# Kernel tuning notes

Measured on AMD Instinct MI355X. Metric: run time of the kernel, lower is better.

## Reference

```python
import jax, jax.numpy as jnp
import numpy as np

B, S, IN, H, NH, PF, L = 8, 1024, 256, 1024, 16, 4096, 6
HD = H // NH
EPS = 1e-5


def _layernorm(x, g, b):
    m = jnp.mean(x, axis=-1, keepdims=True)
    v = jnp.mean((x - m) ** 2, axis=-1, keepdims=True)
    return (x - m) * jax.lax.rsqrt(v + EPS) * g + b


def setup_inputs() -> dict:
    key = jax.random.key(0)
    ks = iter(jax.random.split(key, 40))
    sd = 0.02
    inp = {
        "input_x": jax.random.normal(next(ks), (B, S, IN), jnp.float32),
        "emb_W": jax.random.normal(next(ks), (IN, H), jnp.float32) * sd,
        "emb_b": jnp.zeros((H,), jnp.float32),
        "pos_tab": jax.random.normal(next(ks), (S, H), jnp.float32) * sd,
        "Wq": jax.random.normal(next(ks), (L, H, H), jnp.float32) * sd,
        "bq": jnp.zeros((L, H), jnp.float32),
        "Wk": jax.random.normal(next(ks), (L, H, H), jnp.float32) * sd,
        "bk": jnp.zeros((L, H), jnp.float32),
        "Wv": jax.random.normal(next(ks), (L, H, H), jnp.float32) * sd,
        "bv": jnp.zeros((L, H), jnp.float32),
        "Wo": jax.random.normal(next(ks), (L, H, H), jnp.float32) * sd,
        "bo": jnp.zeros((L, H), jnp.float32),
        "ln1_g": jnp.ones((L, H), jnp.float32),
        "ln1_b": jnp.zeros((L, H), jnp.float32),
        "W1": jax.random.normal(next(ks), (L, H, PF), jnp.float32) * sd,
        "b1": jnp.zeros((L, PF), jnp.float32),
        "W2": jax.random.normal(next(ks), (L, PF, H), jnp.float32) * sd,
        "b2": jnp.zeros((L, H), jnp.float32),
        "ln2_g": jnp.ones((L, H), jnp.float32),
        "ln2_b": jnp.zeros((L, H), jnp.float32),
    }
    return inp


def _encoder(input_x, emb_W, emb_b, pos_tab, Wq, bq, Wk, bk, Wv, bv, Wo, bo,
             ln1_g, ln1_b, W1, b1, W2, b2, ln2_g, ln2_b):
    scale = jnp.sqrt(jnp.float32(H))  # module scales by sqrt(hidden_size)
    x = (input_x @ emb_W + emb_b) * scale + pos_tab[None, :, :]  # [B,S,H]

    def layer(x, p):
        wq, bq_, wk, bk_, wv, bv_, wo, bo_, g1, be1, w1, b1_, w2, b2_, g2, be2 = p
        q = (x @ wq + bq_).reshape(B, S, NH, HD).transpose(0, 2, 1, 3)  # bhsd
        k = (x @ wk + bk_).reshape(B, S, NH, HD).transpose(0, 2, 1, 3)
        v = (x @ wv + bv_).reshape(B, S, NH, HD).transpose(0, 2, 1, 3)
        energy = jnp.einsum("bhqd,bhkd->bhqk", q, k) / scale  # NOTE: /sqrt(H)
        attn = jax.nn.softmax(energy, axis=-1)
        o = jnp.einsum("bhqk,bhkd->bhqd", attn, v)
        o = o.transpose(0, 2, 1, 3).reshape(B, S, H) @ wo + bo_
        x = _layernorm(x + o, g1, be1)
        f = jax.nn.relu(x @ w1 + b1_) @ w2 + b2_
        x = _layernorm(x + f, g2, be2)
        return x, None

    params = (Wq, bq, Wk, bk, Wv, bv, Wo, bo, ln1_g, ln1_b, W1, b1, W2, b2, ln2_g, ln2_b)
    x, _ = jax.lax.scan(layer, x, params)
    return x


def reference(input_x, emb_W, emb_b, pos_tab, Wq, bq, Wk, bk, Wv, bv, Wo, bo,
              ln1_g, ln1_b, W1, b1, W2, b2, ln2_g, ln2_b):
    return _encoder(input_x, emb_W, emb_b, pos_tab, Wq, bq, Wk, bk, Wv, bv,
                    Wo, bo, ln1_g, ln1_b, W1, b1, W2, b2, ln2_g, ln2_b)
```

## Files before the change

kernel.cpp:

```cpp
#include <hip/hip_runtime.h>

#define HDIM 1024
#define BB 8
#define SS 1024
#define NHEAD 16
#define PFF 4096
#define NLAYER 6
#define MM (BB*SS)

typedef __attribute__((ext_vector_type(8))) short bf16x8_t;
typedef __attribute__((ext_vector_type(4))) float f32x4_t;
typedef __attribute__((ext_vector_type(16))) float f32x16_t;

static __device__ __forceinline__ unsigned short f2b(float f) {
  unsigned int u = __float_as_uint(f);
  u += 0x7fffu + ((u >> 16) & 1u);
  return (unsigned short)(u >> 16);
}

static __device__ __forceinline__ unsigned pkbf(float lo, float hi) {
  unsigned r;
  asm("v_cvt_pk_bf16_f32 %0, %1, %2" : "=v"(r) : "v"(lo), "v"(hi));
  return r;
}

static __device__ __forceinline__ bf16x8_t mk8(unsigned a, unsigned b, unsigned c, unsigned d) {
  union { unsigned u[4]; bf16x8_t v; } x;
  x.u[0] = a; x.u[1] = b; x.u[2] = c; x.u[3] = d;
  return x.v;
}

static __device__ __forceinline__ void gload16(const void* g, void* l) {
  __builtin_amdgcn_global_load_lds((__attribute__((address_space(1))) void*)g,
                                   (__attribute__((address_space(3))) void*)l, 16, 0, 0);
}

template<int N>
static __device__ __forceinline__ void vwait() {
  asm volatile("s_waitcnt vmcnt(%0)" :: "n"(N) : "memory");
}

static __device__ __forceinline__ void bar() {
  asm volatile("" ::: "memory");
  __builtin_amdgcn_s_barrier();
  asm volatile("" ::: "memory");
}

__global__ __launch_bounds__(256) void cvt_bf16(const float* __restrict__ in,
                                                unsigned short* __restrict__ o, int n4) {
  const int i = blockIdx.x * 256 + threadIdx.x;
  if (i < n4) {
    const float4 v = ((const float4*)in)[i];
    ushort4 ob = { f2b(v.x), f2b(v.y), f2b(v.z), f2b(v.w) };
    ((ushort4*)o)[i] = ob;
  }
}

__global__ __launch_bounds__(256) void transpose_bf16(const float* __restrict__ in,
                                                      unsigned short* __restrict__ outT,
                                                      int R, int C) {
  __shared__ float tile[32][33];
  const int c0 = blockIdx.x * 32, r0 = blockIdx.y * 32;
  const int tx = threadIdx.x, ty = threadIdx.y;
#pragma unroll
  for (int i = 0; i < 4; ++i)
    tile[ty + 8*i][tx] = in[(size_t)(r0 + ty + 8*i) * C + c0 + tx];
  __syncthreads();
#pragma unroll
  for (int i = 0; i < 4; ++i)
    outT[(size_t)(c0 + ty + 8*i) * R + r0 + tx] = f2b(tile[tx][ty + 8*i]);
}

__global__ __launch_bounds__(256) void vtrans(const unsigned short* __restrict__ qkv,
                                              unsigned short* __restrict__ vt) {
  __shared__ unsigned short tile[32][34];
  const int s0 = blockIdx.x * 32;
  const int by = blockIdx.y;
  const int bh = by >> 1, dt = by & 1;
  const int b = bh >> 4, h = bh & 15;
  const int tx = threadIdx.x, ty = threadIdx.y;
  const unsigned short* src = qkv + ((size_t)(b * 1024 + s0)) * 3072 + 2048 + h * 64 + dt * 32;
#pragma unroll
  for (int i = 0; i < 4; ++i)
    tile[ty + 8*i][tx] = src[(size_t)(ty + 8*i) * 3072 + tx];
  __syncthreads();
  unsigned short* dst = vt + (size_t)(bh * 64 + dt * 32) * 1024 + s0;
#pragma unroll
  for (int i = 0; i < 4; ++i)
    dst[(size_t)(ty + 8*i) * 1024 + tx] = tile[tx][ty + 8*i];
}

__global__ __launch_bounds__(256) void concat_bias(const float* __restrict__ bq,
                                                   const float* __restrict__ bk,
                                                   const float* __restrict__ bv,
                                                   float* __restrict__ o) {
  const int i = blockIdx.x * 256 + threadIdx.x;
  o[i] = (i < 1024) ? bq[i] : ((i < 2048) ? bk[i - 1024] : bv[i - 2048]);
}

template<int BN, bool BIAS, bool RELU, bool RESID, bool EMB, bool WF32, bool WBF16>
__global__ __launch_bounds__(512, 2) void gemm2c(
    const unsigned short* __restrict__ A,
    const unsigned short* __restrict__ Bt,
    const float* __restrict__ bias,
    const float* __restrict__ resid,
    const float* __restrict__ pos,
    float* __restrict__ outf,
    unsigned short* __restrict__ outb,
    int M, int N, int K) {
  constexpr int NJ = BN / 64;
  constexpr int WCN = BN / 4;
  constexpr int BUFSZ = 32768 + BN * 128;
  __shared__ __align__(1024) char smem[2 * BUFSZ];
  const int t = threadIdx.x, lane = t & 63, w = t >> 6;
  const int wr = w >> 2, wc = w & 3;

  int flat = blockIdx.x + gridDim.x * blockIdx.y;
  const int cpx = (gridDim.x * gridDim.y) >> 3;
  flat = (flat & 7) * cpx + (flat >> 3);
  const int m0 = (flat / gridDim.x) * 256;
  const int n0 = (flat % gridDim.x) * BN;

  const f32x4_t z = {0.f, 0.f, 0.f, 0.f};
  f32x4_t acc[8][NJ];
#pragma unroll
  for (int i = 0; i < 8; ++i)
#pragma unroll
    for (int j = 0; j < NJ; ++j) acc[i][j] = z;

  auto stageA = [&](int i, int kt, int buf) {
    const int chunk = i * 8 + w;
    const int byteoff = chunk * 1024 + lane * 16;
    const int row = byteoff >> 7;
    const int scb = (byteoff & 127) ^ ((row & 7) << 4);
    gload16((const char*)A + ((size_t)(m0 + row) * K + (kt << 6)) * 2 + scb,
            smem + buf * BUFSZ + chunk * 1024);
  };
  auto stageB = [&](int i, int kt, int buf) {
    const int chunk = i * 8 + w;
    const int byteoff = chunk * 1024 + lane * 16;
    const int row = byteoff >> 7;
    const int scb = (byteoff & 127) ^ ((row & 7) << 4);
    gload16((const char*)Bt + ((size_t)(n0 + row) * K + (kt << 6)) * 2 + scb,
            smem + buf * BUFSZ + 32768 + chunk * 1024);
  };
  auto readA = [&](const char* ab, int fi, int ks) {
    const int row = wr * 128 + fi * 16 + (lane & 15);
    const int cb = ks * 64 + ((lane >> 4) << 4);
    return *(const bf16x8_t*)(ab + row * 128 + (cb ^ ((row & 7) << 4)));
  };
  auto readB = [&](const char* bb, int j, int ks) {
    const int row = wc * WCN + j * 16 + (lane & 15);
    const int cb = ks * 64 + ((lane >> 4) << 4);
    return *(const bf16x8_t*)(bb + row * 128 + (cb ^ ((row & 7) << 4)));
  };

  stageB(0, 0, 0); stageB(1, 0, 0);
  if constexpr (NJ >= 3) stageB(2, 0, 0);
  if constexpr (NJ >= 4) stageB(3, 0, 0);
  stageA(0, 0, 0); stageA(2, 0, 0); stageA(1, 0, 0); stageA(3, 0, 0);

  const int nkt = K >> 6;
  for (int kt = 0; kt < nkt; ++kt) {
    const char* ab = smem + (kt & 1) * BUFSZ;
    const char* bb = ab + 32768;
    const int nb = (kt & 1) ^ 1;
    const bool pf = (kt + 1 < nkt);
    bf16x8_t bfr[NJ][2], af[8][2];

    if constexpr (BN >= 192) {
      vwait<2>(); bar();
      if (pf) { stageB(0, kt + 1, nb); stageB(1, kt + 1, nb); }
#pragma unroll
      for (int j = 0; j < NJ; ++j)
#pragma unroll
        for (int ks = 0; ks < 2; ++ks) bfr[j][ks] = readB(bb, j, ks);
#pragma unroll
      for (int d = 0; d < 4; ++d)
#pragma unroll
        for (int ks = 0; ks < 2; ++ks) af[d][ks] = readA(ab, d, ks);
      __builtin_amdgcn_s_setprio(1);
#pragma unroll
      for (int ks = 0; ks < 2; ++ks)
#pragma unroll
        for (int d = 0; d < 2; ++d)
#pragma unroll
          for (int j = 0; j < NJ; ++j)
            acc[d][j] = __builtin_amdgcn_mfma_f32_16x16x32_bf16(af[d][ks], bfr[j][ks], acc[d][j], 0, 0, 0);
      __builtin_amdgcn_s_setprio(0);
      if (pf) vwait<2>(); else vwait<0>();
      bar();
      if (pf) {
        stageB(2, kt + 1, nb);
        if constexpr (NJ >= 4) stageB(3, kt + 1, nb);
        stageA(0, kt + 1, nb);
      }
#pragma unroll
      for (int d = 4; d < 6; ++d)
#pragma unroll
        for (int ks = 0; ks < 2; ++ks) af[d][ks] = readA(ab, d, ks);
      __builtin_amdgcn_s_setprio(1);
#pragma unroll
      for (int ks = 0; ks < 2; ++ks)
#pragma unroll
        for (int d = 2; d < 4; ++d)
#pragma unroll
          for (int j = 0; j < NJ; ++j)
            acc[d][j] = __builtin_amdgcn_mfma_f32_16x16x32_bf16(af[d][ks], bfr[j][ks], acc[d][j], 0, 0, 0);
      __builtin_amdgcn_s_setprio(0);
      if (pf) stageA(2, kt + 1, nb);
#pragma unroll
      for (int d = 6; d < 8; ++d)
#pragma unroll
        for (int ks = 0; ks < 2; ++ks) af[d][ks] = readA(ab, d, ks);
      __builtin_amdgcn_s_setprio(1);
#pragma unroll
      for (int ks = 0; ks < 2; ++ks)
#pragma unroll
        for (int d = 4; d < 6; ++d)
#pragma unroll
          for (int j = 0; j < NJ; ++j)
            acc[d][j] = __builtin_amdgcn_mfma_f32_16x16x32_bf16(af[d][ks], bfr[j][ks], acc[d][j], 0, 0, 0);
      __builtin_amdgcn_s_setprio(0);
      if (pf) { stageA(1, kt + 1, nb); stageA(3, kt + 1, nb); }
      __builtin_amdgcn_s_setprio(1);
#pragma unroll
      for (int ks = 0; ks < 2; ++ks)
#pragma unroll
        for (int d = 6; d < 8; ++d)
#pragma unroll
          for (int j = 0; j < NJ; ++j)
            acc[d][j] = __builtin_amdgcn_mfma_f32_16x16x32_bf16(af[d][ks], bfr[j][ks], acc[d][j], 0, 0, 0);
      __builtin_amdgcn_s_setprio(0);
    } else {
      vwait<2>(); bar();
      if (pf) { stageB(0, kt + 1, nb); stageB(1, kt + 1, nb); stageA(0, kt + 1, nb); }
#pragma unroll
      for (int j = 0; j < NJ; ++j)
#pragma unroll
        for (int ks = 0; ks < 2; ++ks) bfr[j][ks] = readB(bb, j, ks);
#pragma unroll
      for (int d = 0; d < 4; ++d)
#pragma unroll
        for (int ks = 0; ks < 2; ++ks) af[d][ks] = readA(ab, d, ks);
      __builtin_amdgcn_s_setprio(1);
#pragma unroll
      for (int ks = 0; ks < 2; ++ks)
#pragma unroll
        for (int d = 0; d < 4; ++d)
#pragma unroll
          for (int j = 0; j < NJ; ++j)
            acc[d][j] = __builtin_amdgcn_mfma_f32_16x16x32_bf16(af[d][ks], bfr[j][ks], acc[d][j], 0, 0, 0);
      __builtin_amdgcn_s_setprio(0);
      if (pf) vwait<3>(); else vwait<0>();
      bar();
      if (pf) { stageA(2, kt + 1, nb); stageA(1, kt + 1, nb); stageA(3, kt + 1, nb); }
#pragma unroll
      for (int d = 4; d < 8; ++d)
#pragma unroll
        for (int ks = 0; ks < 2; ++ks) af[d][ks] = readA(ab, d, ks);
      __builtin_amdgcn_s_setprio(1);
#pragma unroll
      for (int ks = 0; ks < 2; ++ks)
#pragma unroll
        for (int d = 4; d < 8; ++d)
#pragma unroll
          for (int j = 0; j < NJ; ++j)
            acc[4 > d ? 0 : d][j] = __builtin_amdgcn_mfma_f32_16x16x32_bf16(af[d][ks], bfr[j][ks], acc[d][j], 0, 0, 0);
      __builtin_amdgcn_s_setprio(0);
    }
  }

#pragma unroll
  for (int i = 0; i < 8; ++i) {
    const int rbase = m0 + wr * 128 + i * 16 + ((lane >> 4) << 2);
#pragma unroll
    for (int j = 0; j < NJ; ++j) {
      const int cc = n0 + wc * WCN + j * 16 + (lane & 15);
      float bv = 0.f;
      if (BIAS) bv = bias[cc];
#pragma unroll
      for (int r = 0; r < 4; ++r) {
        const int row = rbase + r;
        float v = acc[i][j][r] + bv;
        if (EMB)  v = v * 32.f + pos[(size_t)(row & (SS - 1)) * N + cc];
        if (RELU) v = fmaxf(v, 0.f);
        if (RESID) v += resid[(size_t)row * N + cc];
        if (WF32)  outf[(size_t)row * N + cc] = v;
        if (WBF16) outb[(size_t)row * N + cc] = f2b(v);
      }
    }
  }
}

__global__ __launch_bounds__(256) void attn2(
    const unsigned short* __restrict__ qkv,
    const unsigned short* __restrict__ vt,
    unsigned short* __restrict__ O) {
  __shared__ __align__(1024) char smem[2 * 16384];
  const int t = threadIdx.x, lane = t & 63, w = t >> 6;
  const int l31 = lane & 31, lg = lane >> 5;
  const int bh = blockIdx.y;
  const int b = bh >> 4, h = bh & 15;
  const size_t rowb = (size_t)b << 10;
  const int q0 = blockIdx.x * 128 + w * 32;

  bf16x8_t qf[4];
  {
    const unsigned short* Qp = qkv + (rowb + q0 + l31) * 3072 + h * 64 + lg * 8;
#pragma unroll
    for (int dd = 0; dd < 4; ++dd) qf[dd] = *(const bf16x8_t*)(Qp + dd * 16);
  }

  f32x16_t oa0, oa1;
#pragma unroll
  for (int r = 0; r < 16; ++r) { oa0[r] = 0.f; oa1[r] = 0.f; }
  float m_run = -1e30f, l_run = 0.f;
  const float inv32 = 1.f / 32.f;

  const char* kglob = (const char*)qkv + ((size_t)1024 + h * 64) * 2;
  const char* vglob = (const char*)vt + (size_t)bh * 64 * 1024 * 2;

  auto stage = [&](int kt, int buf) {
    char* kbuf = smem + buf * 16384;
    char* vbuf = kbuf + 8192;
#pragma unroll
    for (int i = 0; i < 2; ++i) {
      const int chunk = w * 2 + i;
      const int byteoff = chunk * 1024 + lane * 16;
      const int row = byteoff >> 7;
      const int scb = (byteoff & 127) ^ ((row & 7) << 4);
      gload16(kglob + (size_t)(rowb + kt * 64 + row) * 6144 + scb, kbuf + chunk * 1024);
      gload16(vglob + ((size_t)row * 1024 + kt * 64) * 2 + scb,    vbuf + chunk * 1024);
    }
  };

  stage(0, 0);
  for (int kt = 0; kt < 16; ++kt) {
    const int cb = kt & 1;
    __syncthreads();
    if (kt < 15) stage(kt + 1, cb ^ 1);
    const char* kbuf = smem + cb * 16384;
    const char* vbuf = kbuf + 8192;

    f32x16_t p0, p1;
#pragma unroll
    for (int r = 0; r < 16; ++r) { p0[r] = 0.f; p1[r] = 0.f; }
    __builtin_amdgcn_s_setprio(1);
#pragma unroll
    for (int dd = 0; dd < 4; ++dd) {
      {
        const int row = l31;
        const int col = (dd * 32 + (lg << 4)) ^ ((row & 7) << 4);
        bf16x8_t kf = *(const bf16x8_t*)(kbuf + row * 128 + col);
        p0 = __builtin_amdgcn_mfma_f32_32x32x16_bf16(kf, qf[dd], p0, 0, 0, 0);
      }
      {
        const int row = 32 + l31;
        const int col = (dd * 32 + (lg << 4)) ^ ((row & 7) << 4);
        bf16x8_t kf = *(const bf16x8_t*)(kbuf + row * 128 + col);
        p1 = __builtin_amdgcn_mfma_f32_32x32x16_bf16(kf, qf[dd], p1, 0, 0, 0);
      }
    }
    __builtin_amdgcn_s_setprio(0);

    float mx = p0[0];
#pragma unroll
    for (int r = 1; r < 16; ++r) mx = fmaxf(mx, p0[r]);
#pragma unroll
    for (int r = 0; r < 16; ++r) mx = fmaxf(mx, p1[r]);
    mx = fmaxf(mx, __shfl_xor(mx, 32));
    const float mn = fmaxf(m_run, mx * inv32);
    const float fr = __expf(m_run - mn);
    m_run = mn;
    float sum = 0.f;
#pragma unroll
    for (int r = 0; r < 16; ++r) { const float e = __expf(p0[r] * inv32 - mn); p0[r] = e; sum += e; }
#pragma unroll
    for (int r = 0; r < 16; ++r) { const float e = __expf(p1[r] * inv32 - mn); p1[r] = e; sum += e; }
    sum += __shfl_xor(sum, 32);
    l_run = l_run * fr + sum;
#pragma unroll
    for (int r = 0; r < 16; ++r) { oa0[r] *= fr; oa1[r] *= fr; }

    const unsigned A0 = pkbf(p0[0], p0[1]),  B0 = pkbf(p0[2], p0[3]);
    const unsigned C0 = pkbf(p0[4], p0[5]),  D0 = pkbf(p0[6], p0[7]);
    const unsigned E0 = pkbf(p0[8], p0[9]),  F0 = pkbf(p0[10], p0[11]);
    const unsigned G0 = pkbf(p0[12], p0[13]), H0 = pkbf(p0[14], p0[15]);
    const unsigned A1 = pkbf(p1[0], p1[1]),  B1 = pkbf(p1[2], p1[3]);
    const unsigned C1 = pkbf(p1[4], p1[5]),  D1 = pkbf(p1[6], p1[7]);
    const unsigned E1 = pkbf(p1[8], p1[9]),  F1 = pkbf(p1[10], p1[11]);
    const unsigned G1 = pkbf(p1[12], p1[13]), H1 = pkbf(p1[14], p1[15]);
    const unsigned sA0 = __shfl_xor((int)A0, 32), sB0 = __shfl_xor((int)B0, 32);
    const unsigned sC0 = __shfl_xor((int)C0, 32), sD0 = __shfl_xor((int)D0, 32);
    const unsigned sE0 = __shfl_xor((int)E0, 32), sF0 = __shfl_xor((int)F0, 32);
    const unsigned sG0 = __shfl_xor((int)G0, 32), sH0 = __shfl_xor((int)H0, 32);
    const unsigned sA1 = __shfl_xor((int)A1, 32), sB1 = __shfl_xor((int)B1, 32);
    const unsigned sC1 = __shfl_xor((int)C1, 32), sD1 = __shfl_xor((int)D1, 32);
    const unsigned sE1 = __shfl_xor((int)E1, 32), sF1 = __shfl_xor((int)F1, 32);
    const unsigned sG1 = __shfl_xor((int)G1, 32), sH1 = __shfl_xor((int)H1, 32);
    const bool hi = (lg != 0);
    bf16x8_t pf[4];
    pf[0] = hi ? mk8(sC0, sD0, C0, D0) : mk8(A0, B0, sA0, sB0);
    pf[1] = hi ? mk8(sG0, sH0, G0, H0) : mk8(E0, F0, sE0, sF0);
    pf[2] = hi ? mk8(sC1, sD1, C1, D1) : mk8(A1, B1, sA1, sB1);
    pf[3] = hi ? mk8(sG1, sH1, G1, H1) : mk8(E1, F1, sE1, sF1);

    __builtin_amdgcn_s_setprio(1);
#pragma unroll
    for (int c = 0; c < 4; ++c) {
      {
        const int row = l31;
        const int col = (c * 32 + (lg << 4)) ^ ((row & 7) << 4);
        bf16x8_t vf = *(const bf16x8_t*)(vbuf + row * 128 + col);
        oa0 = __builtin_amdgcn_mfma_f32_32x32x16_bf16(vf, pf[c], oa0, 0, 0, 0);
      }
      {
        const int row = 32 + l31;
        const int col = (c * 32 + (lg << 4)) ^ ((row & 7) << 4);
        bf16x8_t vf = *(const bf16x8_t*)(vbuf + row * 128 + col);
        oa1 = __builtin_amdgcn_mfma_f32_32x32x16_bf16(vf, pf[c], oa1, 0, 0, 0);
      }
    }
    __builtin_amdgcn_s_setprio(0);
  }

  const float inv = 1.f / l_run;
  unsigned short* op = O + (rowb + q0 + l31) * 1024 + h * 64 + (lg << 2);
#pragma unroll
  for (int rg = 0; rg < 4; ++rg) {
    const unsigned u0 = pkbf(oa0[rg * 4 + 0] * inv, oa0[rg * 4 + 1] * inv);
    const unsigned u1 = pkbf(oa0[rg * 4 + 2] * inv, oa0[rg * 4 + 3] * inv);
    uint2 st = { u0, u1 };
    *(uint2*)(op + rg * 8) = st;
    const unsigned v0 = pkbf(oa1[rg * 4 + 0] * inv, oa1[rg * 4 + 1] * inv);
    const unsigned v1 = pkbf(oa1[rg * 4 + 2] * inv, oa1[rg * 4 + 3] * inv);
    uint2 st2 = { v0, v1 };
    *(uint2*)(op + 32 + rg * 8) = st2;
  }
}

__global__ __launch_bounds__(256) void ln_kernel(
    const float* __restrict__ y, const float* __restrict__ g, const float* __restrict__ be,
    float* __restrict__ xf, unsigned short* __restrict__ xb) {
  const int row = blockIdx.x;
  const int t = threadIdx.x;
  const float4 v = ((const float4*)(y + (size_t)row * HDIM))[t];
  float s  = v.x + v.y + v.z + v.w;
  float ss = v.x*v.x + v.y*v.y + v.z*v.z + v.w*v.w;
#pragma unroll
  for (int m = 1; m < 64; m <<= 1) { s += __shfl_xor(s, m); ss += __shfl_xor(ss, m); }
  __shared__ float rs[4], rss[4];
  const int w = t >> 6, lane = t & 63;
  if (lane == 0) { rs[w] = s; rss[w] = ss; }
  __syncthreads();
  s  = rs[0] + rs[1] + rs[2] + rs[3];
  ss = rss[0] + rss[1] + rss[2] + rss[3];
  const float mean = s * (1.f / HDIM);
  const float inv = rsqrtf(ss * (1.f / HDIM) - mean * mean + 1e-5f);
  const int c = t * 4;
  const float4 gg = *(const float4*)(g + c);
  const float4 bb = *(const float4*)(be + c);
  float4 o;
  o.x = (v.x - mean) * inv * gg.x + bb.x;
  o.y = (v.y - mean) * inv * gg.y + bb.y;
  o.z = (v.z - mean) * inv * gg.z + bb.z;
  o.w = (v.w - mean) * inv * gg.w + bb.w;
  ((float4*)(xf + (size_t)row * HDIM))[t] = o;
  ushort4 ob = { f2b(o.x), f2b(o.y), f2b(o.z), f2b(o.w) };
  ((ushort4*)(xb + (size_t)row * HDIM))[t] = ob;
}

extern "C" void kernel_launch(void* const* d_in, const int* in_sizes, int n_in,
                              void* d_out, int out_size, void* d_ws, size_t ws_size,
                              hipStream_t stream) {
  const float* input_x = (const float*)d_in[0];
  const float* emb_W   = (const float*)d_in[1];
  const float* emb_b   = (const float*)d_in[2];
  const float* pos_tab = (const float*)d_in[3];
  const float* Wq  = (const float*)d_in[4];
  const float* bq  = (const float*)d_in[5];
  const float* Wk  = (const float*)d_in[6];
  const float* bk  = (const float*)d_in[7];
  const float* Wv  = (const float*)d_in[8];
  const float* bv  = (const float*)d_in[9];
  const float* Wo  = (const float*)d_in[10];
  const float* bo  = (const float*)d_in[11];
  const float* ln1g = (const float*)d_in[12];
  const float* ln1b = (const float*)d_in[13];
  const float* W1  = (const float*)d_in[14];
  const float* b1  = (const float*)d_in[15];
  const float* W2  = (const float*)d_in[16];
  const float* b2  = (const float*)d_in[17];
  const float* ln2g = (const float*)d_in[18];
  const float* ln2b = (const float*)d_in[19];
  float* out = (float*)d_out;

  char* ws = (char*)d_ws;
  size_t off = 0;
  auto alloc = [&](size_t bytes) {
    char* p = ws + off;
    off += (bytes + 255) & ~(size_t)255;
    return p;
  };
  unsigned short* wqkvT = (unsigned short*)alloc((size_t)3072 * HDIM * 2);
  unsigned short* woT   = (unsigned short*)alloc((size_t)HDIM * HDIM * 2);
  unsigned short* w1T   = (unsigned short*)alloc((size_t)PFF * HDIM * 2);
  unsigned short* w2T   = (unsigned short*)alloc((size_t)HDIM * PFF * 2);
  unsigned short* embWT = (unsigned short*)alloc((size_t)HDIM * 256 * 2);
  float*          bqkv  = (float*)alloc(3072 * 4);
  unsigned short* inb   = (unsigned short*)alloc((size_t)MM * 256 * 2);
  unsigned short* xb    = (unsigned short*)alloc((size_t)MM * HDIM * 2);
  unsigned short* qkvb  = (unsigned short*)alloc((size_t)MM * 3072 * 2);
  unsigned short* vtb   = (unsigned short*)alloc((size_t)MM * HDIM * 2);
  unsigned short* ab    = (unsigned short*)alloc((size_t)MM * HDIM * 2);
  float* y = (float*)alloc((size_t)MM * HDIM * 4);
  unsigned short* hb = qkvb;

  const dim3 blk256(256);
  const dim3 blk512(512);
  const dim3 tblk(32, 8);

  cvt_bf16<<<dim3(MM * 256 / 4 / 256), blk256, 0, stream>>>(input_x, inb, MM * 256 / 4);
  transpose_bf16<<<dim3(HDIM / 32, 256 / 32), tblk, 0, stream>>>(emb_W, embWT, 256, HDIM);

  gemm2c<128, true, false, false, true, true, true><<<dim3(HDIM / 128, MM / 256), blk512, 0, stream>>>(
      inb, embWT, emb_b, nullptr, pos_tab, out, xb, MM, HDIM, 256);

  for (int l = 0; l < NLAYER; ++l) {
    const size_t wofs = (size_t)l * HDIM * HDIM;
    transpose_bf16<<<dim3(32, 32), tblk, 0, stream>>>(Wq + wofs, wqkvT,               HDIM, HDIM);
    transpose_bf16<<<dim3(32, 32), tblk, 0, stream>>>(Wk + wofs, wqkvT + 1024 * 1024, HDIM, HDIM);
    transpose_bf16<<<dim3(32, 32), tblk, 0, stream>>>(Wv + wofs, wqkvT + 2048 * 1024, HDIM, HDIM);
    transpose_bf16<<<dim3(32, 32), tblk, 0, stream>>>(Wo + wofs, woT, HDIM, HDIM);
    transpose_bf16<<<dim3(PFF / 32, HDIM / 32), tblk, 0, stream>>>(
        W1 + (size_t)l * HDIM * PFF, w1T, HDIM, PFF);
    transpose_bf16<<<dim3(HDIM / 32, PFF / 32), tblk, 0, stream>>>(
        W2 + (size_t)l * PFF * HDIM, w2T, PFF, HDIM);
    concat_bias<<<dim3(12), blk256, 0, stream>>>(bq + l * HDIM, bk + l * HDIM, bv + l * HDIM, bqkv);

    gemm2c<192, true, false, false, false, false, true><<<dim3(3072 / 192, MM / 256), blk512, 0, stream>>>(
        xb, wqkvT, bqkv, nullptr, nullptr, nullptr, qkvb, MM, 3072, HDIM);

    vtrans<<<dim3(32, 256), tblk, 0, stream>>>(qkvb, vtb);

    attn2<<<dim3(SS / 128, BB * NHEAD), blk256, 0, stream>>>(qkvb, vtb, ab);

    gemm2c<128, true, false, true, false, true, false><<<dim3(HDIM / 128, MM / 256), blk512, 0, stream>>>(
        ab, woT, bo + l * HDIM, out, nullptr, y, nullptr, MM, HDIM, HDIM);
    ln_kernel<<<dim3(MM), blk256, 0, stream>>>(y, ln1g + l * HDIM, ln1b + l * HDIM, out, xb);

    gemm2c<256, true, true, false, false, false, true><<<dim3(PFF / 256, MM / 256), blk512, 0, stream>>>(
        xb, w1T, b1 + (size_t)l * PFF, nullptr, nullptr, nullptr, hb, MM, PFF, HDIM);
    gemm2c<128, true, false, true, false, true, false><<<dim3(HDIM / 128, MM / 256), blk512, 0, stream>>>(
        hb, w2T, b2 + l * HDIM, out, nullptr, y, nullptr, MM, HDIM, PFF);
    ln_kernel<<<dim3(MM), blk256, 0, stream>>>(y, ln2g + l * HDIM, ln2b + l * HDIM, out, xb);
  }
  (void)in_sizes; (void)n_in; (void)out_size; (void)ws_size;
}
```

Measured before the change: 2.195 ms.

## Add 8-barrier MFMA phase scheduling and store pre-LayerNorm residual in bf16

```diff
diff --git a/kernel.cpp b/kernel.cpp
--- a/kernel.cpp
+++ b/kernel.cpp
@@ -18,6 +18,10 @@
   return (unsigned short)(u >> 16);
 }
 
+static __device__ __forceinline__ float b2f(unsigned short u) {
+  return __uint_as_float(((unsigned)u) << 16);
+}
+
 static __device__ __forceinline__ unsigned pkbf(float lo, float hi) {
   unsigned r;
   asm("v_cvt_pk_bf16_f32 %0, %1, %2" : "=v"(r) : "v"(lo), "v"(hi));
@@ -44,6 +48,11 @@
   asm volatile("" ::: "memory");
   __builtin_amdgcn_s_barrier();
   asm volatile("" ::: "memory");
+}
+
+static __device__ __forceinline__ void lgkm0() {
+  asm volatile("s_waitcnt lgkmcnt(0)" ::: "memory");
+  __builtin_amdgcn_sched_barrier(0);
 }
 
 __global__ __launch_bounds__(256) void cvt_bf16(const float* __restrict__ in,
@@ -99,7 +108,7 @@
 }
 
 template<int BN, bool BIAS, bool RELU, bool RESID, bool EMB, bool WF32, bool WBF16>
-__global__ __launch_bounds__(512, 2) void gemm2c(
+__global__ __launch_bounds__(512, 2) void gemm8b(
     const unsigned short* __restrict__ A,
     const unsigned short* __restrict__ Bt,
     const float* __restrict__ bias,
@@ -179,6 +188,7 @@
       for (int d = 0; d < 4; ++d)
 #pragma unroll
         for (int ks = 0; ks < 2; ++ks) af[d][ks] = readA(ab, d, ks);
+      bar(); lgkm0();
       __builtin_amdgcn_s_setprio(1);
 #pragma unroll
       for (int ks = 0; ks < 2; ++ks)
@@ -188,6 +198,7 @@
           for (int j = 0; j < NJ; ++j)
             acc[d][j] = __builtin_amdgcn_mfma_f32_16x16x32_bf16(af[d][ks], bfr[j][ks], acc[d][j], 0, 0, 0);
       __builtin_amdgcn_s_setprio(0);
+      bar();
       if (pf) vwait<2>(); else vwait<0>();
       bar();
       if (pf) {
@@ -199,6 +210,7 @@
       for (int d = 4; d < 6; ++d)
 #pragma unroll
         for (int ks = 0; ks < 2; ++ks) af[d][ks] = readA(ab, d, ks);
+      bar(); lgkm0();
       __builtin_amdgcn_s_setprio(1);
 #pragma unroll
       for (int ks = 0; ks < 2; ++ks)
@@ -208,11 +220,13 @@
           for (int j = 0; j < NJ; ++j)
             acc[d][j] = __builtin_amdgcn_mfma_f32_16x16x32_bf16(af[d][ks], bfr[j][ks], acc[d][j], 0, 0, 0);
       __builtin_amdgcn_s_setprio(0);
+      bar();
       if (pf) stageA(2, kt + 1, nb);
 #pragma unroll
       for (int d = 6; d < 8; ++d)
 #pragma unroll
         for (int ks = 0; ks < 2; ++ks) af[d][ks] = readA(ab, d, ks);
+      bar(); lgkm0();
       __builtin_amdgcn_s_setprio(1);
 #pragma unroll
       for (int ks = 0; ks < 2; ++ks)
@@ -222,6 +236,7 @@
           for (int j = 0; j < NJ; ++j)
             acc[d][j] = __builtin_amdgcn_mfma_f32_16x16x32_bf16(af[d][ks], bfr[j][ks], acc[d][j], 0, 0, 0);
       __builtin_amdgcn_s_setprio(0);
+      bar();
       if (pf) { stageA(1, kt + 1, nb); stageA(3, kt + 1, nb); }
       __builtin_amdgcn_s_setprio(1);
 #pragma unroll
@@ -243,6 +258,7 @@
       for (int d = 0; d < 4; ++d)
 #pragma unroll
         for (int ks = 0; ks < 2; ++ks) af[d][ks] = readA(ab, d, ks);
+      bar(); lgkm0();
       __builtin_amdgcn_s_setprio(1);
 #pragma unroll
       for (int ks = 0; ks < 2; ++ks)
@@ -252,6 +268,7 @@
           for (int j = 0; j < NJ; ++j)
             acc[d][j] = __builtin_amdgcn_mfma_f32_16x16x32_bf16(af[d][ks], bfr[j][ks], acc[d][j], 0, 0, 0);
       __builtin_amdgcn_s_setprio(0);
+      bar();
       if (pf) vwait<3>(); else vwait<0>();
       bar();
       if (pf) { stageA(2, kt + 1, nb); stageA(1, kt + 1, nb); stageA(3, kt + 1, nb); }
@@ -259,6 +276,7 @@
       for (int d = 4; d < 8; ++d)
 #pragma unroll
         for (int ks = 0; ks < 2; ++ks) af[d][ks] = readA(ab, d, ks);
+      bar(); lgkm0();
       __builtin_amdgcn_s_setprio(1);
 #pragma unroll
       for (int ks = 0; ks < 2; ++ks)
@@ -266,7 +284,7 @@
         for (int d = 4; d < 8; ++d)
 #pragma unroll
           for (int j = 0; j < NJ; ++j)
-            acc[4 > d ? 0 : d][j] = __builtin_amdgcn_mfma_f32_16x16x32_bf16(af[d][ks], bfr[j][ks], acc[d][j], 0, 0, 0);
+            acc[d][j] = __builtin_amdgcn_mfma_f32_16x16x32_bf16(af[d][ks], bfr[j][ks], acc[d][j], 0, 0, 0);
       __builtin_amdgcn_s_setprio(0);
     }
   }
@@ -440,12 +458,14 @@
   }
 }
 
-__global__ __launch_bounds__(256) void ln_kernel(
-    const float* __restrict__ y, const float* __restrict__ g, const float* __restrict__ be,
+__global__ __launch_bounds__(256) void lnb_kernel(
+    const unsigned short* __restrict__ yb, const float* __restrict__ g,
+    const float* __restrict__ be,
     float* __restrict__ xf, unsigned short* __restrict__ xb) {
   const int row = blockIdx.x;
   const int t = threadIdx.x;
-  const float4 v = ((const float4*)(y + (size_t)row * HDIM))[t];
+  const ushort4 u = ((const ushort4*)(yb + (size_t)row * HDIM))[t];
+  float4 v = { b2f(u.x), b2f(u.y), b2f(u.z), b2f(u.w) };
   float s  = v.x + v.y + v.z + v.w;
   float ss = v.x*v.x + v.y*v.y + v.z*v.z + v.w*v.w;
 #pragma unroll
@@ -514,7 +534,7 @@
   unsigned short* qkvb  = (unsigned short*)alloc((size_t)MM * 3072 * 2);
   unsigned short* vtb   = (unsigned short*)alloc((size_t)MM * HDIM * 2);
   unsigned short* ab    = (unsigned short*)alloc((size_t)MM * HDIM * 2);
-  float* y = (float*)alloc((size_t)MM * HDIM * 4);
+  unsigned short* yb    = (unsigned short*)alloc((size_t)MM * HDIM * 2);
   unsigned short* hb = qkvb;
 
   const dim3 blk256(256);
@@ -524,7 +544,7 @@
   cvt_bf16<<<dim3(MM * 256 / 4 / 256), blk256, 0, stream>>>(input_x, inb, MM * 256 / 4);
   transpose_bf16<<<dim3(HDIM / 32, 256 / 32), tblk, 0, stream>>>(emb_W, embWT, 256, HDIM);
 
-  gemm2c<128, true, false, false, true, true, true><<<dim3(HDIM / 128, MM / 256), blk512, 0, stream>>>(
+  gemm8b<128, true, false, false, true, true, true><<<dim3(HDIM / 128, MM / 256), blk512, 0, stream>>>(
       inb, embWT, emb_b, nullptr, pos_tab, out, xb, MM, HDIM, 256);
 
   for (int l = 0; l < NLAYER; ++l) {
@@ -539,22 +559,22 @@
         W2 + (size_t)l * PFF * HDIM, w2T, PFF, HDIM);
     concat_bias<<<dim3(12), blk256, 0, stream>>>(bq + l * HDIM, bk + l * HDIM, bv + l * HDIM, bqkv);
 
-    gemm2c<192, true, false, false, false, false, true><<<dim3(3072 / 192, MM / 256), blk512, 0, stream>>>(
+    gemm8b<192, true, false, false, false, false, true><<<dim3(3072 / 192, MM / 256), blk512, 0, stream>>>(
         xb, wqkvT, bqkv, nullptr, nullptr, nullptr, qkvb, MM, 3072, HDIM);
 
     vtrans<<<dim3(32, 256), tblk, 0, stream>>>(qkvb, vtb);
 
     attn2<<<dim3(SS / 128, BB * NHEAD), blk256, 0, stream>>>(qkvb, vtb, ab);
 
-    gemm2c<128, true, false, true, false, true, false><<<dim3(HDIM / 128, MM / 256), blk512, 0, stream>>>(
-        ab, woT, bo + l * HDIM, out, nullptr, y, nullptr, MM, HDIM, HDIM);
-    ln_kernel<<<dim3(MM), blk256, 0, stream>>>(y, ln1g + l * HDIM, ln1b + l * HDIM, out, xb);
-
-    gemm2c<256, true, true, false, false, false, true><<<dim3(PFF / 256, MM / 256), blk512, 0, stream>>>(
+    gemm8b<128, true, false, true, false, false, true><<<dim3(HDIM / 128, MM / 256), blk512, 0, stream>>>(
+        ab, woT, bo + l * HDIM, out, nullptr, nullptr, yb, MM, HDIM, HDIM);
+    lnb_kernel<<<dim3(MM), blk256, 0, stream>>>(yb, ln1g + l * HDIM, ln1b + l * HDIM, out, xb);
+
+    gemm8b<256, true, true, false, false, false, true><<<dim3(PFF / 256, MM / 256), blk512, 0, stream>>>(
         xb, w1T, b1 + (size_t)l * PFF, nullptr, nullptr, nullptr, hb, MM, PFF, HDIM);
-    gemm2c<128, true, false, true, false, true, false><<<dim3(HDIM / 128, MM / 256), blk512, 0, stream>>>(
-        hb, w2T, b2 + l * HDIM, out, nullptr, y, nullptr, MM, HDIM, PFF);
-    ln_kernel<<<dim3(MM), blk256, 0, stream>>>(y, ln2g + l * HDIM, ln2b + l * HDIM, out, xb);
+    gemm8b<128, true, false, true, false, false, true><<<dim3(HDIM / 128, MM / 256), blk512, 0, stream>>>(
+        hb, w2T, b2 + l * HDIM, out, nullptr, nullptr, yb, MM, HDIM, PFF);
+    lnb_kernel<<<dim3(MM), blk256, 0, stream>>>(yb, ln2g + l * HDIM, ln2b + l * HDIM, out, xb);
   }
   (void)in_sizes; (void)n_in; (void)out_size; (void)ws_size;
 }
```

Measured after the change: 2.235 ms. About the same (+1.8%).
